# Kernel tuning notes

Measured on AMD Instinct MI355X. Metric: run time of the kernel, lower is better.

Reference implementation:

```python
import jax, jax.numpy as jnp
import numpy as np

FUTURE_K = 32
NEG_INF = -1e9  # finite large-negative to keep softmax NaN-free on fully-masked rows


def setup_inputs() -> dict:
    key = jax.random.key(0)
    hidden_states = jax.random.normal(key, (4, 2048, 1024), dtype=jnp.float32)
    return {"hidden_states": hidden_states}


def reference(hidden_states) -> jnp.ndarray:
    # Faithful vectorized version of FutureEncoder(summary_method='attention').
    # For each t: window = h[:, t+1 : min(t+1+K, S)], scores = h_t @ window^T,
    # summary_t = softmax(scores) @ window. t = S-1 (empty window) stays zero.
    B, S, D = hidden_states.shape
    offs = jnp.arange(1, FUTURE_K + 1)                 # [K]
    idx = jnp.arange(S)[:, None] + offs[None, :]       # [S, K] future indices t+1..t+K
    valid = idx < S                                     # [S, K]
    idx_c = jnp.minimum(idx, S - 1)
    fw = hidden_states[:, idx_c, :]                     # [B, S, K, D] gathered windows
    scores = jnp.einsum('bsd,bskd->bsk', hidden_states, fw)
    scores = jnp.where(valid[None, :, :], scores, NEG_INF)
    w = jax.nn.softmax(scores, axis=-1)                 # [B, S, K]
    w = jnp.where(valid[None, :, :], w, 0.0)
    out = jnp.einsum('bsk,bskd->bsd', w, fw)            # [B, S, D]
    any_valid = valid.any(axis=-1)                      # [S]; False only at t = S-1
    return jnp.where(any_valid[None, :, None], out, 0.0)
```

## Files before the change

### kernel.cpp

```cpp
#include <hip/hip_runtime.h>
#include <math.h>


constexpr int S_CONST = 2048;
constexpr int D = 1024;
constexpr int G = 16;
constexpr int NTOK = 8192;
constexpr int JP = 49;
constexpr int TB = 8;

typedef short bf16x8 __attribute__((ext_vector_type(8)));
typedef float f32x4  __attribute__((ext_vector_type(4)));
typedef unsigned int u32x4 __attribute__((ext_vector_type(4)));

__device__ inline void cvt8(float4 x0, float4 x1, bf16x8& hi, bf16x8& lo) {
    float xs[8] = {x0.x, x0.y, x0.z, x0.w, x1.x, x1.y, x1.z, x1.w};
    u32x4 hv, lv;
    #pragma unroll
    for (int p = 0; p < 4; ++p) {
        float a = xs[2 * p], b = xs[2 * p + 1];
        unsigned hp;
        asm("v_cvt_pk_bf16_f32 %0, %1, %2" : "=v"(hp) : "v"(a), "v"(b));
        float ha = __builtin_bit_cast(float, hp << 16);
        float hb = __builtin_bit_cast(float, hp & 0xffff0000u);
        float la = a - ha, lb = b - hb;
        unsigned lp;
        asm("v_cvt_pk_bf16_f32 %0, %1, %2" : "=v"(lp) : "v"(la), "v"(lb));
        hv[p] = hp; lv[p] = lp;
    }
    hi = __builtin_bit_cast(bf16x8, hv);
    lo = __builtin_bit_cast(bf16x8, lv);
}

__global__ __launch_bounds__(256, 2)
void scores_kernel(const float* __restrict__ h, float* __restrict__ wmg) {
    __shared__ float sc[4 * G * JP];

    int bid = blockIdx.x, nblk = gridDim.x, lb = bid;
    if ((nblk & 7) == 0) {
        int per = nblk >> 3;
        lb = (bid & 7) * per + (bid >> 3);
    }

    const int tid  = threadIdx.x;
    const int w    = tid >> 6;
    const int lane = tid & 63;
    const int t0   = lb * G;
    const int s0   = t0 & (S_CONST - 1);
    const int jlim = (S_CONST - 2) - s0;

    {
        const int d0   = w * 256;
        const int mrow = lane & 15;
        const int q8   = (lane >> 4) * 8;

        const float* A = h + (size_t)(t0 + mrow) * D + d0 + q8;
        int r0 = min(t0 +  1 + mrow, NTOK - 1);
        int r1 = min(t0 + 17 + mrow, NTOK - 1);
        int r2 = min(t0 + 33 + mrow, NTOK - 1);
        const float* B0 = h + (size_t)r0 * D + d0 + q8;
        const float* B1 = h + (size_t)r1 * D + d0 + q8;
        const float* B2 = h + (size_t)r2 * D + d0 + q8;

        f32x4 acc[3] = {{0,0,0,0},{0,0,0,0},{0,0,0,0}};

        float4 xa0 = *(const float4*)(A),  xa1 = *(const float4*)(A + 4);
        float4 x00 = *(const float4*)(B0), x01 = *(const float4*)(B0 + 4);
        float4 x10 = *(const float4*)(B1), x11 = *(const float4*)(B1 + 4);
        float4 x20 = *(const float4*)(B2), x21 = *(const float4*)(B2 + 4);

        #pragma unroll
        for (int kk = 0; kk < 8; ++kk) {
            float4 na0, na1, n00, n01, n10, n11, n20, n21;
            if (kk < 7) {
                const int o = (kk + 1) * 32;
                na0 = *(const float4*)(A  + o); na1 = *(const float4*)(A  + o + 4);
                n00 = *(const float4*)(B0 + o); n01 = *(const float4*)(B0 + o + 4);
                n10 = *(const float4*)(B1 + o); n11 = *(const float4*)(B1 + o + 4);
                n20 = *(const float4*)(B2 + o); n21 = *(const float4*)(B2 + o + 4);
            }

            bf16x8 ah, al, bh, bl;
            cvt8(xa0, xa1, ah, al);

            cvt8(x00, x01, bh, bl);
            acc[0] = __builtin_amdgcn_mfma_f32_16x16x32_bf16(ah, bh, acc[0], 0, 0, 0);
            acc[0] = __builtin_amdgcn_mfma_f32_16x16x32_bf16(ah, bl, acc[0], 0, 0, 0);
            acc[0] = __builtin_amdgcn_mfma_f32_16x16x32_bf16(al, bh, acc[0], 0, 0, 0);

            cvt8(x10, x11, bh, bl);
            acc[1] = __builtin_amdgcn_mfma_f32_16x16x32_bf16(ah, bh, acc[1], 0, 0, 0);
            acc[1] = __builtin_amdgcn_mfma_f32_16x16x32_bf16(ah, bl, acc[1], 0, 0, 0);
            acc[1] = __builtin_amdgcn_mfma_f32_16x16x32_bf16(al, bh, acc[1], 0, 0, 0);

            cvt8(x20, x21, bh, bl);
            acc[2] = __builtin_amdgcn_mfma_f32_16x16x32_bf16(ah, bh, acc[2], 0, 0, 0);
            acc[2] = __builtin_amdgcn_mfma_f32_16x16x32_bf16(ah, bl, acc[2], 0, 0, 0);
            acc[2] = __builtin_amdgcn_mfma_f32_16x16x32_bf16(al, bh, acc[2], 0, 0, 0);

            if (kk < 7) {
                xa0 = na0; xa1 = na1;
                x00 = n00; x01 = n01;
                x10 = n10; x11 = n11;
                x20 = n20; x21 = n21;
            }
        }

        #pragma unroll
        for (int t = 0; t < 3; ++t) {
            #pragma unroll
            for (int r = 0; r < 4; ++r) {
                int m = (lane >> 4) * 4 + r;
                int j = t * 16 + (lane & 15);
                sc[(w * G + m) * JP + j] = acc[t][r];
            }
        }
    }
    __syncthreads();

    {
        const int i   = tid >> 4;
        const int sub = tid & 15;

        float v[3];
        #pragma unroll
        for (int c = 0; c < 3; ++c) {
            int j = sub + c * 16;
            float s = sc[(0 * G + i) * JP + j] + sc[(1 * G + i) * JP + j]
                    + sc[(2 * G + i) * JP + j] + sc[(3 * G + i) * JP + j];
            bool valid = (j >= i) && (j <= i + 31) && (j <= jlim);
            v[c] = valid ? s : -1e9f;
        }
        float mx = fmaxf(v[0], fmaxf(v[1], v[2]));
        #pragma unroll
        for (int d = 1; d < 16; d <<= 1) mx = fmaxf(mx, __shfl_xor(mx, d, 16));

        float e[3];
        float sum = 0.f;
        #pragma unroll
        for (int c = 0; c < 3; ++c) { e[c] = __expf(v[c] - mx); sum += e[c]; }
        #pragma unroll
        for (int d = 1; d < 16; d <<= 1) sum += __shfl_xor(sum, d, 16);

        const bool any = (mx > -5e8f);
        const float inv = any ? (1.0f / sum) : 0.f;

        float* wrow = wmg + (size_t)(t0 + i) * 32;
        #pragma unroll
        for (int c = 0; c < 3; ++c) {
            int j = sub + c * 16;
            int k = j - i;
            if (k >= 0 && k < 32)
                wrow[k] = (j <= jlim) ? e[c] * inv : 0.f;
        }
    }
}

__global__ __launch_bounds__(256, 4)
void pv_kernel(const float* __restrict__ h, const float* __restrict__ wm,
               float* __restrict__ out) {
    __shared__ float lw[TB * 32];

    int bid = blockIdx.x, nblk = gridDim.x, lb = bid;
    if ((nblk & 7) == 0) {
        int per = nblk >> 3;
        lb = (bid & 7) * per + (bid >> 3);
    }
    const int i0   = lb * TB;
    const int tid  = threadIdx.x;
    const int doff = tid * 4;

    lw[tid] = wm[(size_t)i0 * 32 + tid];
    __syncthreads();

    float4 acc[TB] = {};
    float4 wv[TB];

    #pragma unroll
    for (int rr = 0; rr < TB + 31; ++rr) {
        int r = min(i0 + 1 + rr, NTOK - 1);
        float4 f = *(const float4*)(h + (size_t)r * D + doff);
        #pragma unroll
        for (int t = 0; t < TB; ++t) {
            const int k = rr - t;
            if (k >= 0 && k < 32) {
                if ((k & 3) == 0)
                    wv[t] = *(const float4*)(&lw[t * 32 + k]);
                const float wt = ((k & 3) == 0) ? wv[t].x :
                                 ((k & 3) == 1) ? wv[t].y :
                                 ((k & 3) == 2) ? wv[t].z : wv[t].w;
                acc[t].x += wt * f.x;
                acc[t].y += wt * f.y;
                acc[t].z += wt * f.z;
                acc[t].w += wt * f.w;
            }
        }
    }

    #pragma unroll
    for (int t = 0; t < TB; ++t)
        *(float4*)(out + (size_t)(i0 + t) * D + doff) = acc[t];
}

extern "C" void kernel_launch(void* const* d_in, const int* in_sizes, int n_in,
                              void* d_out, int out_size, void* d_ws, size_t ws_size,
                              hipStream_t stream) {
    const float* h = (const float*)d_in[0];
    float* out = (float*)d_out;
    float* wm = (float*)d_ws;
    const int ntok = in_sizes[0] / D;

    scores_kernel<<<ntok / G, 256, 0, stream>>>(h, wm);
    pv_kernel<<<ntok / TB, 256, 0, stream>>>(h, wm, out);
}
```

Baseline: 104.9 us.

## Stage score-kernel rows through double-buffered swizzled LDS with direct global-to-LDS loads

The scores kernel now loads the 49 needed rows (16 query rows plus 33 future rows) into LDS once per 128-column chunk. The buffer is double-buffered and XOR-swizzled, and filled with global_load_lds where available. Previously each wave read A and B rows straight from global memory, and overlapping rows were fetched redundantly. Work is split across 6 waves (3 score tiles by 2 K-halves), and partial sums are reduced through a small shared array. This trades extra LDS use (about 50KB) and a barrier per chunk for less duplicated global traffic, which may lower occupancy.

After: 108.6 us. 1.04x slower.

```diff
diff --git a/kernel.cpp b/kernel.cpp
--- a/kernel.cpp
+++ b/kernel.cpp
@@ -6,7 +6,6 @@
 constexpr int D = 1024;
 constexpr int G = 16;
 constexpr int NTOK = 8192;
-constexpr int JP = 49;
 constexpr int TB = 8;
 
 typedef short bf16x8 __attribute__((ext_vector_type(8)));
@@ -32,9 +31,21 @@
     lo = __builtin_bit_cast(bf16x8, lv);
 }
 
-__global__ __launch_bounds__(256, 2)
+#if __has_builtin(__builtin_amdgcn_global_load_lds)
+#define HAVE_GLDS 1
+__device__ inline void gload_lds16(const float* gp, float* lp) {
+    __builtin_amdgcn_global_load_lds(
+        (const __attribute__((address_space(1))) void*)gp,
+        (__attribute__((address_space(3))) void*)lp, 16, 0, 0);
+}
+#else
+#define HAVE_GLDS 0
+#endif
+
+__global__ __launch_bounds__(384)
 void scores_kernel(const float* __restrict__ h, float* __restrict__ wmg) {
-    __shared__ float sc[4 * G * JP];
+    __shared__ float buf[2][49 * 128];
+    __shared__ float sc6[6][16][17];
 
     int bid = blockIdx.x, nblk = gridDim.x, lb = bid;
     if ((nblk & 7) == 0) {
@@ -49,76 +60,71 @@
     const int s0   = t0 & (S_CONST - 1);
     const int jlim = (S_CONST - 2) - s0;
 
-    {
-        const int d0   = w * 256;
-        const int mrow = lane & 15;
-        const int q8   = (lane >> 4) * 8;
-
-        const float* A = h + (size_t)(t0 + mrow) * D + d0 + q8;
-        int r0 = min(t0 +  1 + mrow, NTOK - 1);
-        int r1 = min(t0 + 17 + mrow, NTOK - 1);
-        int r2 = min(t0 + 33 + mrow, NTOK - 1);
-        const float* B0 = h + (size_t)r0 * D + d0 + q8;
-        const float* B1 = h + (size_t)r1 * D + d0 + q8;
-        const float* B2 = h + (size_t)r2 * D + d0 + q8;
-
-        f32x4 acc[3] = {{0,0,0,0},{0,0,0,0},{0,0,0,0}};
-
-        float4 xa0 = *(const float4*)(A),  xa1 = *(const float4*)(A + 4);
-        float4 x00 = *(const float4*)(B0), x01 = *(const float4*)(B0 + 4);
-        float4 x10 = *(const float4*)(B1), x11 = *(const float4*)(B1 + 4);
-        float4 x20 = *(const float4*)(B2), x21 = *(const float4*)(B2 + 4);
-
-        #pragma unroll
-        for (int kk = 0; kk < 8; ++kk) {
-            float4 na0, na1, n00, n01, n10, n11, n20, n21;
-            if (kk < 7) {
-                const int o = (kk + 1) * 32;
-                na0 = *(const float4*)(A  + o); na1 = *(const float4*)(A  + o + 4);
-                n00 = *(const float4*)(B0 + o); n01 = *(const float4*)(B0 + o + 4);
-                n10 = *(const float4*)(B1 + o); n11 = *(const float4*)(B1 + o + 4);
-                n20 = *(const float4*)(B2 + o); n21 = *(const float4*)(B2 + o + 4);
+    const int tile = w >> 1;
+    const int kp   = w & 1;
+    const int mq   = lane >> 4;
+    const int mr   = lane & 15;
+
+    auto stage = [&](int pp, int c) {
+        #pragma unroll
+        for (int r = 0; r < 5; ++r) {
+            int s = r * 384 + w * 64 + lane;
+            if (s < 49 * 32) {
+                int row = s >> 5;
+                int li  = s & 31;
+                int grow = min(t0 + row, NTOK - 1);
+                int swz  = ((li * 16) ^ ((row & 7) << 4)) >> 2;
+                const float* gp = h + (size_t)grow * D + c * 128 + swz;
+#if HAVE_GLDS
+                float* lp = &buf[pp][(r * 384 + w * 64) * 4];
+                gload_lds16(gp, lp);
+#else
+                *(float4*)&buf[pp][s * 4] = *(const float4*)gp;
+#endif
             }
-
-            bf16x8 ah, al, bh, bl;
-            cvt8(xa0, xa1, ah, al);
-
-            cvt8(x00, x01, bh, bl);
-            acc[0] = __builtin_amdgcn_mfma_f32_16x16x32_bf16(ah, bh, acc[0], 0, 0, 0);
-            acc[0] = __builtin_amdgcn_mfma_f32_16x16x32_bf16(ah, bl, acc[0], 0, 0, 0);
-            acc[0] = __builtin_amdgcn_mfma_f32_16x16x32_bf16(al, bh, acc[0], 0, 0, 0);
-
-            cvt8(x10, x11, bh, bl);
-            acc[1] = __builtin_amdgcn_mfma_f32_16x16x32_bf16(ah, bh, acc[1], 0, 0, 0);
-            acc[1] = __builtin_amdgcn_mfma_f32_16x16x32_bf16(ah, bl, acc[1], 0, 0, 0);
-            acc[1] = __builtin_amdgcn_mfma_f32_16x16x32_bf16(al, bh, acc[1], 0, 0, 0);
-
-            cvt8(x20, x21, bh, bl);
-            acc[2] = __builtin_amdgcn_mfma_f32_16x16x32_bf16(ah, bh, acc[2], 0, 0, 0);
-            acc[2] = __builtin_amdgcn_mfma_f32_16x16x32_bf16(ah, bl, acc[2], 0, 0, 0);
-            acc[2] = __builtin_amdgcn_mfma_f32_16x16x32_bf16(al, bh, acc[2], 0, 0, 0);
-
-            if (kk < 7) {
-                xa0 = na0; xa1 = na1;
-                x00 = n00; x01 = n01;
-                x10 = n10; x11 = n11;
-                x20 = n20; x21 = n21;
-            }
-        }
-
-        #pragma unroll
-        for (int t = 0; t < 3; ++t) {
-            #pragma unroll
-            for (int r = 0; r < 4; ++r) {
-                int m = (lane >> 4) * 4 + r;
-                int j = t * 16 + (lane & 15);
-                sc[(w * G + m) * JP + j] = acc[t][r];
-            }
-        }
-    }
+        }
+    };
+
+    f32x4 acc = {0, 0, 0, 0};
+
+    stage(0, 0);
     __syncthreads();
 
-    {
+    for (int c = 0; c < 8; ++c) {
+        if (c < 7) stage((c + 1) & 1, c + 1);
+        const float* bc = buf[c & 1];
+
+        #pragma unroll
+        for (int kh = 0; kh < 2; ++kh) {
+            const int ks = kp * 2 + kh;
+            const int f0 = ks * 32 + mq * 8;
+
+            const int Xa = (mr & 7) << 2;
+            float4 a0 = *(const float4*)&bc[mr * 128 + ((f0)     ^ Xa)];
+            float4 a1 = *(const float4*)&bc[mr * 128 + ((f0 + 4) ^ Xa)];
+            bf16x8 ah, al;
+            cvt8(a0, a1, ah, al);
+
+            const int rb = 1 + tile * 16 + mr;
+            const int Xb = (rb & 7) << 2;
+            float4 b0 = *(const float4*)&bc[rb * 128 + ((f0)     ^ Xb)];
+            float4 b1 = *(const float4*)&bc[rb * 128 + ((f0 + 4) ^ Xb)];
+            bf16x8 bh, bl;
+            cvt8(b0, b1, bh, bl);
+
+            acc = __builtin_amdgcn_mfma_f32_16x16x32_bf16(ah, bh, acc, 0, 0, 0);
+            acc = __builtin_amdgcn_mfma_f32_16x16x32_bf16(ah, bl, acc, 0, 0, 0);
+            acc = __builtin_amdgcn_mfma_f32_16x16x32_bf16(al, bh, acc, 0, 0, 0);
+        }
+        __syncthreads();
+    }
+
+    #pragma unroll
+    for (int r = 0; r < 4; ++r)
+        sc6[w][mq * 4 + r][mr] = acc[r];
+    __syncthreads();
+
+    if (tid < 256) {
         const int i   = tid >> 4;
         const int sub = tid & 15;
 
@@ -126,8 +132,7 @@
         #pragma unroll
         for (int c = 0; c < 3; ++c) {
             int j = sub + c * 16;
-            float s = sc[(0 * G + i) * JP + j] + sc[(1 * G + i) * JP + j]
-                    + sc[(2 * G + i) * JP + j] + sc[(3 * G + i) * JP + j];
+            float s = sc6[c * 2 + 0][i][sub] + sc6[c * 2 + 1][i][sub];
             bool valid = (j >= i) && (j <= i + 31) && (j <= jlim);
             v[c] = valid ? s : -1e9f;
         }
@@ -210,6 +215,6 @@
     float* wm = (float*)d_ws;
     const int ntok = in_sizes[0] / D;
 
-    scores_kernel<<<ntok / G, 256, 0, stream>>>(h, wm);
+    scores_kernel<<<ntok / G, 384, 0, stream>>>(h, wm);
     pv_kernel<<<ntok / TB, 256, 0, stream>>>(h, wm, out);
 }
```

## Fuse scores and weighted-sum kernels into one block-local kernel

Applied to the files above, without the earlier changes.

Merges the scores/softmax kernel and the PV kernel into a single 512-thread kernel. Each block handles 32 tokens and keeps the softmax weights in shared memory instead of writing them to a global workspace and launching a second kernel. The PV stage is restructured so each wave computes 4 output rows over the full D, reusing each loaded future row across the 4 rows. This removes a launch and the workspace round-trip. In exchange there are only 256 blocks, so parallelism drops, and the PV loop has fewer independent loads in flight per thread.

After: 125.0 us. 19.2% more time.

```diff
diff --git a/kernel.cpp b/kernel.cpp
--- a/kernel.cpp
+++ b/kernel.cpp
@@ -4,10 +4,10 @@
 
 constexpr int S_CONST = 2048;
 constexpr int D = 1024;
-constexpr int G = 16;
+constexpr int G = 32;
 constexpr int NTOK = 8192;
 constexpr int JP = 49;
-constexpr int TB = 8;
+constexpr int WQ = 33;
 
 typedef short bf16x8 __attribute__((ext_vector_type(8)));
 typedef float f32x4  __attribute__((ext_vector_type(4)));
@@ -32,9 +32,11 @@
     lo = __builtin_bit_cast(bf16x8, lv);
 }
 
-__global__ __launch_bounds__(256, 2)
-void scores_kernel(const float* __restrict__ h, float* __restrict__ wmg) {
-    __shared__ float sc[4 * G * JP];
+__global__ __launch_bounds__(512)
+void future_encoder_kernel(const float* __restrict__ h,
+                           float* __restrict__ out) {
+    __shared__ float sc[8 * 16 * JP];
+    __shared__ float wm[G * WQ];
 
     int bid = blockIdx.x, nblk = gridDim.x, lb = bid;
     if ((nblk & 7) == 0) {
@@ -46,18 +48,19 @@
     const int w    = tid >> 6;
     const int lane = tid & 63;
     const int t0   = lb * G;
-    const int s0   = t0 & (S_CONST - 1);
-    const int jlim = (S_CONST - 2) - s0;
 
     {
-        const int d0   = w * 256;
+        const int th   = w >> 2;
+        const int ds   = w & 3;
+        const int d0   = ds * 256;
         const int mrow = lane & 15;
         const int q8   = (lane >> 4) * 8;
-
-        const float* A = h + (size_t)(t0 + mrow) * D + d0 + q8;
-        int r0 = min(t0 +  1 + mrow, NTOK - 1);
-        int r1 = min(t0 + 17 + mrow, NTOK - 1);
-        int r2 = min(t0 + 33 + mrow, NTOK - 1);
+        const int tb   = t0 + 16 * th;
+
+        const float* A = h + (size_t)(tb + mrow) * D + d0 + q8;
+        int r0 = min(tb +  1 + mrow, NTOK - 1);
+        int r1 = min(tb + 17 + mrow, NTOK - 1);
+        int r2 = min(tb + 33 + mrow, NTOK - 1);
         const float* B0 = h + (size_t)r0 * D + d0 + q8;
         const float* B1 = h + (size_t)r1 * D + d0 + q8;
         const float* B2 = h + (size_t)r2 * D + d0 + q8;
@@ -112,7 +115,7 @@
             for (int r = 0; r < 4; ++r) {
                 int m = (lane >> 4) * 4 + r;
                 int j = t * 16 + (lane & 15);
-                sc[(w * G + m) * JP + j] = acc[t][r];
+                sc[(w * 16 + m) * JP + j] = acc[t][r];
             }
         }
     }
@@ -121,14 +124,20 @@
     {
         const int i   = tid >> 4;
         const int sub = tid & 15;
+        const int th2 = i >> 4;
+        const int m   = i & 15;
+        const int sb  = (t0 + 16 * th2) & (S_CONST - 1);
+        const int jl  = (S_CONST - 2) - sb;
 
         float v[3];
         #pragma unroll
         for (int c = 0; c < 3; ++c) {
             int j = sub + c * 16;
-            float s = sc[(0 * G + i) * JP + j] + sc[(1 * G + i) * JP + j]
-                    + sc[(2 * G + i) * JP + j] + sc[(3 * G + i) * JP + j];
-            bool valid = (j >= i) && (j <= i + 31) && (j <= jlim);
+            float s = sc[((th2 * 4 + 0) * 16 + m) * JP + j]
+                    + sc[((th2 * 4 + 1) * 16 + m) * JP + j]
+                    + sc[((th2 * 4 + 2) * 16 + m) * JP + j]
+                    + sc[((th2 * 4 + 3) * 16 + m) * JP + j];
+            bool valid = (j >= m) && (j <= m + 31) && (j <= jl);
             v[c] = valid ? s : -1e9f;
         }
         float mx = fmaxf(v[0], fmaxf(v[1], v[2]));
@@ -145,61 +154,50 @@
         const bool any = (mx > -5e8f);
         const float inv = any ? (1.0f / sum) : 0.f;
 
-        float* wrow = wmg + (size_t)(t0 + i) * 32;
         #pragma unroll
         for (int c = 0; c < 3; ++c) {
             int j = sub + c * 16;
-            int k = j - i;
-            if (k >= 0 && k < 32)
-                wrow[k] = (j <= jlim) ? e[c] * inv : 0.f;
-        }
-    }
-}
-
-__global__ __launch_bounds__(256, 4)
-void pv_kernel(const float* __restrict__ h, const float* __restrict__ wm,
-               float* __restrict__ out) {
-    __shared__ float lw[TB * 32];
-
-    int bid = blockIdx.x, nblk = gridDim.x, lb = bid;
-    if ((nblk & 7) == 0) {
-        int per = nblk >> 3;
-        lb = (bid & 7) * per + (bid >> 3);
-    }
-    const int i0   = lb * TB;
-    const int tid  = threadIdx.x;
-    const int doff = tid * 4;
-
-    lw[tid] = wm[(size_t)i0 * 32 + tid];
+            int q = j - m;
+            bool valid = (j >= m) && (j <= m + 31) && (j <= jl);
+            if (q >= 0 && q < 32)
+                wm[i * WQ + q] = valid ? e[c] * inv : 0.f;
+        }
+    }
     __syncthreads();
 
-    float4 acc[TB] = {};
-    float4 wv[TB];
-
-    #pragma unroll
-    for (int rr = 0; rr < TB + 31; ++rr) {
-        int r = min(i0 + 1 + rr, NTOK - 1);
-        float4 f = *(const float4*)(h + (size_t)r * D + doff);
-        #pragma unroll
-        for (int t = 0; t < TB; ++t) {
-            const int k = rr - t;
-            if (k >= 0 && k < 32) {
-                if ((k & 3) == 0)
-                    wv[t] = *(const float4*)(&lw[t * 32 + k]);
-                const float wt = ((k & 3) == 0) ? wv[t].x :
-                                 ((k & 3) == 1) ? wv[t].y :
-                                 ((k & 3) == 2) ? wv[t].z : wv[t].w;
-                acc[t].x += wt * f.x;
-                acc[t].y += wt * f.y;
-                acc[t].z += wt * f.z;
-                acc[t].w += wt * f.w;
-            }
-        }
-    }
-
-    #pragma unroll
-    for (int t = 0; t < TB; ++t)
-        *(float4*)(out + (size_t)(i0 + t) * D + doff) = acc[t];
+    {
+        const int i0   = w * 4;
+        const int doff = lane * 4;
+
+        float4 a0[4] = {}, a1[4] = {}, a2[4] = {}, a3[4] = {};
+
+        for (int rr = 0; rr <= 34; ++rr) {
+            int r = min(t0 + 1 + i0 + rr, NTOK - 1);
+            const float* fp = h + (size_t)r * D + doff;
+            const float w0 = (rr <= 31)            ? wm[(i0 + 0) * WQ + rr]     : 0.f;
+            const float w1 = (rr >= 1 && rr <= 32) ? wm[(i0 + 1) * WQ + rr - 1] : 0.f;
+            const float w2 = (rr >= 2 && rr <= 33) ? wm[(i0 + 2) * WQ + rr - 2] : 0.f;
+            const float w3 = (rr >= 3)             ? wm[(i0 + 3) * WQ + rr - 3] : 0.f;
+            #pragma unroll
+            for (int c = 0; c < 4; ++c) {
+                float4 f = *(const float4*)(fp + c * 256);
+                a0[c].x += w0 * f.x; a0[c].y += w0 * f.y; a0[c].z += w0 * f.z; a0[c].w += w0 * f.w;
+                a1[c].x += w1 * f.x; a1[c].y += w1 * f.y; a1[c].z += w1 * f.z; a1[c].w += w1 * f.w;
+                a2[c].x += w2 * f.x; a2[c].y += w2 * f.y; a2[c].z += w2 * f.z; a2[c].w += w2 * f.w;
+                a3[c].x += w3 * f.x; a3[c].y += w3 * f.y; a3[c].z += w3 * f.z; a3[c].w += w3 * f.w;
+            }
+        }
+
+        float* o0 = out + (size_t)(t0 + i0) * D + doff;
+        #pragma unroll
+        for (int c = 0; c < 4; ++c) *(float4*)(o0 + 0 * D + c * 256) = a0[c];
+        #pragma unroll
+        for (int c = 0; c < 4; ++c) *(float4*)(o0 + 1 * D + c * 256) = a1[c];
+        #pragma unroll
+        for (int c = 0; c < 4; ++c) *(float4*)(o0 + 2 * D + c * 256) = a2[c];
+        #pragma unroll
+        for (int c = 0; c < 4; ++c) *(float4*)(o0 + 3 * D + c * 256) = a3[c];
+    }
 }
 
 extern "C" void kernel_launch(void* const* d_in, const int* in_sizes, int n_in,
@@ -207,9 +205,7 @@
                               hipStream_t stream) {
     const float* h = (const float*)d_in[0];
     float* out = (float*)d_out;
-    float* wm = (float*)d_ws;
     const int ntok = in_sizes[0] / D;
-
-    scores_kernel<<<ntok / G, 256, 0, stream>>>(h, wm);
-    pv_kernel<<<ntok / TB, 256, 0, stream>>>(h, wm, out);
+    const int blocks = ntok / G;
+    future_encoder_kernel<<<blocks, 512, 0, stream>>>(h, out);
 }
```

## Split score reduction over D halves and move softmax into PV kernel

Applied to the files above, without the earlier changes.

The scores kernel now splits the D dimension into two halves across twice as many blocks and writes raw partial score rows (48 per token per half) to the workspace. The softmax, masking and summing of the two partials move into the start of the PV kernel, which builds the weights in shared memory. This doubles the parallelism of the scores stage and halves each block's reduction loop. In exchange it adds extra workspace traffic for the partial scores and a short serial prologue in the PV kernel. Launch bounds hints are also dropped from both kernels.

After: 107.8 us. +2.7%, slower.

```diff
diff --git a/kernel.cpp b/kernel.cpp
--- a/kernel.cpp
+++ b/kernel.cpp
@@ -32,8 +32,8 @@
     lo = __builtin_bit_cast(bf16x8, lv);
 }
 
-__global__ __launch_bounds__(256, 2)
-void scores_kernel(const float* __restrict__ h, float* __restrict__ wmg) {
+__global__ __launch_bounds__(256)
+void scores_kernel(const float* __restrict__ h, float* __restrict__ ps) {
     __shared__ float sc[4 * G * JP];
 
     int bid = blockIdx.x, nblk = gridDim.x, lb = bid;
@@ -41,16 +41,16 @@
         int per = nblk >> 3;
         lb = (bid & 7) * per + (bid >> 3);
     }
+    const int tg = lb & 511;
+    const int dh = lb >> 9;
 
     const int tid  = threadIdx.x;
     const int w    = tid >> 6;
     const int lane = tid & 63;
-    const int t0   = lb * G;
-    const int s0   = t0 & (S_CONST - 1);
-    const int jlim = (S_CONST - 2) - s0;
+    const int t0   = tg * G;
 
     {
-        const int d0   = w * 256;
+        const int d0   = dh * 512 + w * 128;
         const int mrow = lane & 15;
         const int q8   = (lane >> 4) * 8;
 
@@ -70,9 +70,9 @@
         float4 x20 = *(const float4*)(B2), x21 = *(const float4*)(B2 + 4);
 
         #pragma unroll
-        for (int kk = 0; kk < 8; ++kk) {
+        for (int kk = 0; kk < 4; ++kk) {
             float4 na0, na1, n00, n01, n10, n11, n20, n21;
-            if (kk < 7) {
+            if (kk < 3) {
                 const int o = (kk + 1) * 32;
                 na0 = *(const float4*)(A  + o); na1 = *(const float4*)(A  + o + 4);
                 n00 = *(const float4*)(B0 + o); n01 = *(const float4*)(B0 + o + 4);
@@ -98,7 +98,7 @@
             acc[2] = __builtin_amdgcn_mfma_f32_16x16x32_bf16(ah, bl, acc[2], 0, 0, 0);
             acc[2] = __builtin_amdgcn_mfma_f32_16x16x32_bf16(al, bh, acc[2], 0, 0, 0);
 
-            if (kk < 7) {
+            if (kk < 3) {
                 xa0 = na0; xa1 = na1;
                 x00 = n00; x01 = n01;
                 x10 = n10; x11 = n11;
@@ -121,45 +121,21 @@
     {
         const int i   = tid >> 4;
         const int sub = tid & 15;
-
-        float v[3];
+        float* prow = ps + ((size_t)dh * NTOK + t0 + i) * 48;
         #pragma unroll
         for (int c = 0; c < 3; ++c) {
             int j = sub + c * 16;
             float s = sc[(0 * G + i) * JP + j] + sc[(1 * G + i) * JP + j]
                     + sc[(2 * G + i) * JP + j] + sc[(3 * G + i) * JP + j];
-            bool valid = (j >= i) && (j <= i + 31) && (j <= jlim);
-            v[c] = valid ? s : -1e9f;
-        }
-        float mx = fmaxf(v[0], fmaxf(v[1], v[2]));
-        #pragma unroll
-        for (int d = 1; d < 16; d <<= 1) mx = fmaxf(mx, __shfl_xor(mx, d, 16));
-
-        float e[3];
-        float sum = 0.f;
-        #pragma unroll
-        for (int c = 0; c < 3; ++c) { e[c] = __expf(v[c] - mx); sum += e[c]; }
-        #pragma unroll
-        for (int d = 1; d < 16; d <<= 1) sum += __shfl_xor(sum, d, 16);
-
-        const bool any = (mx > -5e8f);
-        const float inv = any ? (1.0f / sum) : 0.f;
-
-        float* wrow = wmg + (size_t)(t0 + i) * 32;
-        #pragma unroll
-        for (int c = 0; c < 3; ++c) {
-            int j = sub + c * 16;
-            int k = j - i;
-            if (k >= 0 && k < 32)
-                wrow[k] = (j <= jlim) ? e[c] * inv : 0.f;
-        }
-    }
-}
-
-__global__ __launch_bounds__(256, 4)
-void pv_kernel(const float* __restrict__ h, const float* __restrict__ wm,
+            prow[j] = s;
+        }
+    }
+}
+
+__global__ __launch_bounds__(256)
+void pv_kernel(const float* __restrict__ h, const float* __restrict__ ps,
                float* __restrict__ out) {
-    __shared__ float lw[TB * 32];
+    __shared__ float wm[TB * 32];
 
     int bid = blockIdx.x, nblk = gridDim.x, lb = bid;
     if ((nblk & 7) == 0) {
@@ -168,11 +144,41 @@
     }
     const int i0   = lb * TB;
     const int tid  = threadIdx.x;
+
+    if (tid < 128) {
+        const int i   = tid >> 4;
+        const int sub = tid & 15;
+        const int tok = i0 + i;
+        const int iA  = tok & 15;
+        const int sp  = tok & (S_CONST - 1);
+        const int qmx = (S_CONST - 2) - sp;
+
+        const float* p0 = ps + (size_t)tok * 48 + iA;
+        const float* p1 = ps + ((size_t)NTOK + tok) * 48 + iA;
+
+        float v0 = p0[sub]      + p1[sub];
+        float v1 = p0[sub + 16] + p1[sub + 16];
+        v0 = (sub      <= qmx) ? v0 : -1e9f;
+        v1 = (sub + 16 <= qmx) ? v1 : -1e9f;
+
+        float mx = fmaxf(v0, v1);
+        #pragma unroll
+        for (int d = 1; d < 16; d <<= 1) mx = fmaxf(mx, __shfl_xor(mx, d, 16));
+
+        float e0 = __expf(v0 - mx), e1 = __expf(v1 - mx);
+        float sum = e0 + e1;
+        #pragma unroll
+        for (int d = 1; d < 16; d <<= 1) sum += __shfl_xor(sum, d, 16);
+
+        const bool any = (mx > -5e8f);
+        const float inv = any ? (1.0f / sum) : 0.f;
+
+        wm[i * 32 + sub]      = (sub      <= qmx) ? e0 * inv : 0.f;
+        wm[i * 32 + sub + 16] = (sub + 16 <= qmx) ? e1 * inv : 0.f;
+    }
+    __syncthreads();
+
     const int doff = tid * 4;
-
-    lw[tid] = wm[(size_t)i0 * 32 + tid];
-    __syncthreads();
-
     float4 acc[TB] = {};
     float4 wv[TB];
 
@@ -185,7 +191,7 @@
             const int k = rr - t;
             if (k >= 0 && k < 32) {
                 if ((k & 3) == 0)
-                    wv[t] = *(const float4*)(&lw[t * 32 + k]);
+                    wv[t] = *(const float4*)(&wm[t * 32 + k]);
                 const float wt = ((k & 3) == 0) ? wv[t].x :
                                  ((k & 3) == 1) ? wv[t].y :
                                  ((k & 3) == 2) ? wv[t].z : wv[t].w;
@@ -207,9 +213,9 @@
                               hipStream_t stream) {
     const float* h = (const float*)d_in[0];
     float* out = (float*)d_out;
-    float* wm = (float*)d_ws;
+    float* ps = (float*)d_ws;
     const int ntok = in_sizes[0] / D;
 
-    scores_kernel<<<ntok / G, 256, 0, stream>>>(h, wm);
-    pv_kernel<<<ntok / TB, 256, 0, stream>>>(h, wm, out);
-}
+    scores_kernel<<<(ntok / G) * 2, 256, 0, stream>>>(h, ps);
+    pv_kernel<<<ntok / TB, 256, 0, stream>>>(h, ps, out);
+}
```
